# Kernel optimization log

Measured on AMD Instinct MI355X. Metric: run time of the kernel, lower is better.

## Reference

```python
import jax, jax.numpy as jnp
import numpy as np

B, N, E, H = 2, 256, 256, 768


def setup_inputs() -> dict:
    key = jax.random.key(0)
    ks = jax.random.split(key, 9)
    s_e = 1.0 / np.sqrt(E)
    s_h = 1.0 / np.sqrt(H)
    return {
        "x": jax.random.normal(ks[0], (B, N, E), dtype=jnp.float32),
        "Wq": jax.random.uniform(ks[1], (E, H), jnp.float32, -s_e, s_e),
        "bq": jax.random.uniform(ks[2], (H,), jnp.float32, -s_e, s_e),
        "Wk": jax.random.uniform(ks[3], (E, H), jnp.float32, -s_e, s_e),
        "bk": jax.random.uniform(ks[4], (H,), jnp.float32, -s_e, s_e),
        "Wv": jax.random.uniform(ks[5], (E, H), jnp.float32, -s_e, s_e),
        "bv": jax.random.uniform(ks[6], (H,), jnp.float32, -s_e, s_e),
        "we": jax.random.uniform(ks[7], (H,), jnp.float32, -s_h, s_h),
        "be": jax.random.uniform(ks[8], (), jnp.float32, -s_h, s_h),
    }


def reference(x, Wq, bq, Wk, bk, Wv, bv, we, be):
    # Projections: [B,N,H]
    q = x @ Wq + bq
    k = x @ Wk + bk
    v = x @ Wv + bv
    # Per (i,j): q_i + k_j + v_j  (key and value both broadcast over query axis)
    kv = k + v  # [B,N,H]
    # energy: [B,N,N] = leaky_relu(q_i + kv_j) . we + be
    energy = jnp.einsum(
        "bijh,h->bij",
        jax.nn.leaky_relu(q[:, :, None, :] + kv[:, None, :, :], negative_slope=0.01),
        we,
    ) + be
    attn = jax.nn.softmax(energy, axis=-1)  # softmax over keys j
    return jnp.einsum("bij,bjh->bih", attn, v)  # [B,N,H]
```

## Files before the change

### kernel.cpp

```cpp
#include <hip/hip_runtime.h>

#define B 2
#define N 256
#define E 256
#define H 768
#define H4 (H / 4)

__global__ __launch_bounds__(256) void proj_kernel(
    const float* __restrict__ x,
    const float* __restrict__ Wq, const float* __restrict__ bq,
    const float* __restrict__ Wk, const float* __restrict__ bk,
    const float* __restrict__ Wv, const float* __restrict__ bv,
    float* __restrict__ q, float* __restrict__ v, float4* __restrict__ kvT)
{
    __shared__ float  xs[E][8];
    __shared__ float4 red[8][4][64];

    const int t    = threadIdx.x;
    const int lane = t & 63;
    const int rg   = t >> 6;
    const int type = blockIdx.x / 192;
    const int bid  = blockIdx.x % 192;
    const int ct   = bid >> 6;
    const int rt   = bid & 63;
    const int r0   = rt * 8;
    const int c    = ct * 256 + lane * 4;

    {
        float4 lo, hi;
        lo.x = x[(r0 + 0) * E + t]; lo.y = x[(r0 + 1) * E + t];
        lo.z = x[(r0 + 2) * E + t]; lo.w = x[(r0 + 3) * E + t];
        hi.x = x[(r0 + 4) * E + t]; hi.y = x[(r0 + 5) * E + t];
        hi.z = x[(r0 + 6) * E + t]; hi.w = x[(r0 + 7) * E + t];
        *(float4*)&xs[t][0] = lo;
        *(float4*)&xs[t][4] = hi;
    }

    float4 bias;
    if (type == 0)       bias = *(const float4*)(bq + c);
    else if (type == 2)  bias = *(const float4*)(bv + c);
    else {
        const float4 p = *(const float4*)(bk + c);
        const float4 r = *(const float4*)(bv + c);
        bias.x = p.x + r.x; bias.y = p.y + r.y; bias.z = p.z + r.z; bias.w = p.w + r.w;
    }
    __syncthreads();

    const int e0 = rg * 64;
    float4 a0 = {0,0,0,0}, a1 = a0, a2 = a0, a3 = a0, a4 = a0, a5 = a0, a6 = a0, a7 = a0;

#define PROJ_STEP(ee, wv)                                                     \
    { const float4 xA = *(const float4*)&xs[ee][0];                           \
      const float4 xB = *(const float4*)&xs[ee][4];                           \
      a0.x = fmaf(xA.x, wv.x, a0.x); a0.y = fmaf(xA.x, wv.y, a0.y);           \
      a0.z = fmaf(xA.x, wv.z, a0.z); a0.w = fmaf(xA.x, wv.w, a0.w);           \
      a1.x = fmaf(xA.y, wv.x, a1.x); a1.y = fmaf(xA.y, wv.y, a1.y);           \
      a1.z = fmaf(xA.y, wv.z, a1.z); a1.w = fmaf(xA.y, wv.w, a1.w);           \
      a2.x = fmaf(xA.z, wv.x, a2.x); a2.y = fmaf(xA.z, wv.y, a2.y);           \
      a2.z = fmaf(xA.z, wv.z, a2.z); a2.w = fmaf(xA.z, wv.w, a2.w);           \
      a3.x = fmaf(xA.w, wv.x, a3.x); a3.y = fmaf(xA.w, wv.y, a3.y);           \
      a3.z = fmaf(xA.w, wv.z, a3.z); a3.w = fmaf(xA.w, wv.w, a3.w);           \
      a4.x = fmaf(xB.x, wv.x, a4.x); a4.y = fmaf(xB.x, wv.y, a4.y);           \
      a4.z = fmaf(xB.x, wv.z, a4.z); a4.w = fmaf(xB.x, wv.w, a4.w);           \
      a5.x = fmaf(xB.y, wv.x, a5.x); a5.y = fmaf(xB.y, wv.y, a5.y);           \
      a5.z = fmaf(xB.y, wv.z, a5.z); a5.w = fmaf(xB.y, wv.w, a5.w);           \
      a6.x = fmaf(xB.z, wv.x, a6.x); a6.y = fmaf(xB.z, wv.y, a6.y);           \
      a6.z = fmaf(xB.z, wv.z, a6.z); a6.w = fmaf(xB.z, wv.w, a6.w);           \
      a7.x = fmaf(xB.w, wv.x, a7.x); a7.y = fmaf(xB.w, wv.y, a7.y);           \
      a7.z = fmaf(xB.w, wv.z, a7.z); a7.w = fmaf(xB.w, wv.w, a7.w); }

    if (type == 1) {
        const float4* Wkp = (const float4*)(Wk + c);
        const float4* Wvp = (const float4*)(Wv + c);
        float4 k0 = Wkp[(e0 + 0) * H4], k1 = Wkp[(e0 + 1) * H4];
        float4 k2 = Wkp[(e0 + 2) * H4], k3 = Wkp[(e0 + 3) * H4];
        float4 u0 = Wvp[(e0 + 0) * H4], u1 = Wvp[(e0 + 1) * H4];
        float4 u2 = Wvp[(e0 + 2) * H4], u3 = Wvp[(e0 + 3) * H4];
        float4 s0, s1, s2, s3;
        s0.x=k0.x+u0.x; s0.y=k0.y+u0.y; s0.z=k0.z+u0.z; s0.w=k0.w+u0.w;
        s1.x=k1.x+u1.x; s1.y=k1.y+u1.y; s1.z=k1.z+u1.z; s1.w=k1.w+u1.w;
        s2.x=k2.x+u2.x; s2.y=k2.y+u2.y; s2.z=k2.z+u2.z; s2.w=k2.w+u2.w;
        s3.x=k3.x+u3.x; s3.y=k3.y+u3.y; s3.z=k3.z+u3.z; s3.w=k3.w+u3.w;
        int e = e0;
        #pragma unroll 1
        for (; e < e0 + 60; e += 4) {
            float4 nk0 = Wkp[(e + 4) * H4], nk1 = Wkp[(e + 5) * H4];
            float4 nk2 = Wkp[(e + 6) * H4], nk3 = Wkp[(e + 7) * H4];
            float4 nu0 = Wvp[(e + 4) * H4], nu1 = Wvp[(e + 5) * H4];
            float4 nu2 = Wvp[(e + 6) * H4], nu3 = Wvp[(e + 7) * H4];
            PROJ_STEP(e    , s0);
            PROJ_STEP(e + 1, s1);
            PROJ_STEP(e + 2, s2);
            PROJ_STEP(e + 3, s3);
            s0.x=nk0.x+nu0.x; s0.y=nk0.y+nu0.y; s0.z=nk0.z+nu0.z; s0.w=nk0.w+nu0.w;
            s1.x=nk1.x+nu1.x; s1.y=nk1.y+nu1.y; s1.z=nk1.z+nu1.z; s1.w=nk1.w+nu1.w;
            s2.x=nk2.x+nu2.x; s2.y=nk2.y+nu2.y; s2.z=nk2.z+nu2.z; s2.w=nk2.w+nu2.w;
            s3.x=nk3.x+nu3.x; s3.y=nk3.y+nu3.y; s3.z=nk3.z+nu3.z; s3.w=nk3.w+nu3.w;
        }
        PROJ_STEP(e    , s0);
        PROJ_STEP(e + 1, s1);
        PROJ_STEP(e + 2, s2);
        PROJ_STEP(e + 3, s3);
    } else {
        const float* W = (type == 0) ? Wq : Wv;
        const float4* Wp = (const float4*)(W + c);
        float4 w0 = Wp[(e0 + 0) * H4], w1 = Wp[(e0 + 1) * H4];
        float4 w2 = Wp[(e0 + 2) * H4], w3 = Wp[(e0 + 3) * H4];
        int e = e0;
        #pragma unroll 1
        for (; e < e0 + 60; e += 4) {
            float4 n0 = Wp[(e + 4) * H4], n1 = Wp[(e + 5) * H4];
            float4 n2 = Wp[(e + 6) * H4], n3 = Wp[(e + 7) * H4];
            PROJ_STEP(e    , w0);
            PROJ_STEP(e + 1, w1);
            PROJ_STEP(e + 2, w2);
            PROJ_STEP(e + 3, w3);
            w0 = n0; w1 = n1; w2 = n2; w3 = n3;
        }
        PROJ_STEP(e    , w0);
        PROJ_STEP(e + 1, w1);
        PROJ_STEP(e + 2, w2);
        PROJ_STEP(e + 3, w3);
    }
#undef PROJ_STEP

    red[0][rg][lane] = a0; red[1][rg][lane] = a1;
    red[2][rg][lane] = a2; red[3][rg][lane] = a3;
    red[4][rg][lane] = a4; red[5][rg][lane] = a5;
    red[6][rg][lane] = a6; red[7][rg][lane] = a7;
    __syncthreads();

    #pragma unroll
    for (int ri = 0; ri < 2; ++ri) {
        const int r = 2 * rg + ri;
        const float4 p0 = red[r][0][lane], p1 = red[r][1][lane];
        const float4 p2 = red[r][2][lane], p3 = red[r][3][lane];
        float4 s;
        s.x = ((p0.x + p1.x) + (p2.x + p3.x)) + bias.x;
        s.y = ((p0.y + p1.y) + (p2.y + p3.y)) + bias.y;
        s.z = ((p0.z + p1.z) + (p2.z + p3.z)) + bias.z;
        s.w = ((p0.w + p1.w) + (p2.w + p3.w)) + bias.w;
        const int row = r0 + r;
        if (type == 0) {
            *(float4*)(q + row * H + c) = s;
        } else if (type == 2) {
            *(float4*)(v + row * H + c) = s;
        } else {
            const int b = row >> 8, n = row & 255;
            kvT[(b * H4 + (c >> 2)) * N + n] = s;
        }
    }
}

__global__ __launch_bounds__(512) void energy_kernel(
    const float* __restrict__ q, const float4* __restrict__ kvT,
    const float* __restrict__ we, const float* __restrict__ be_p,
    float* __restrict__ eout)
{
    __shared__ float qs[8][H];
    __shared__ float wes[H];
    __shared__ float pE[8][8][64];

    const int t    = threadIdx.x;
    const int jl   = t & 63;
    const int hq   = t >> 6;
    const int row0 = (blockIdx.x >> 2) * 8;
    const int j0   = (blockIdx.x & 3) * 64;
    const int b    = row0 >> 8;

    for (int i = t; i < H; i += 512) {
        wes[i] = we[i];
        #pragma unroll
        for (int r = 0; r < 8; ++r) qs[r][i] = q[(row0 + r) * H + i];
    }
    __syncthreads();

    const float4* kvp = kvT + (size_t)b * H4 * N + (j0 + jl);
    const int base = hq * 24;

    float acc[8] = {0.f, 0.f, 0.f, 0.f, 0.f, 0.f, 0.f, 0.f};

#define ESTEP8(idx, kvv)                                                      \
    { const float4 ww = *(const float4*)&wes[(idx) * 4];                      \
      _Pragma("unroll")                                                       \
      for (int r = 0; r < 8; ++r) {                                           \
          const float4 qa = *(const float4*)&qs[r][(idx) * 4];                \
          float s;                                                            \
          s = qa.x + kvv.x; acc[r] = fmaf(fmaxf(s, 0.01f * s), ww.x, acc[r]); \
          s = qa.y + kvv.y; acc[r] = fmaf(fmaxf(s, 0.01f * s), ww.y, acc[r]); \
          s = qa.z + kvv.z; acc[r] = fmaf(fmaxf(s, 0.01f * s), ww.z, acc[r]); \
          s = qa.w + kvv.w; acc[r] = fmaf(fmaxf(s, 0.01f * s), ww.w, acc[r]); \
      } }

    float4 k0 = kvp[(base + 0) * N], k1 = kvp[(base + 1) * N];
    float4 k2 = kvp[(base + 2) * N], k3 = kvp[(base + 3) * N];
    int it = 0;
    #pragma unroll 1
    for (; it < 20; it += 4) {
        float4 n0 = kvp[(base + it + 4) * N], n1 = kvp[(base + it + 5) * N];
        float4 n2 = kvp[(base + it + 6) * N], n3 = kvp[(base + it + 7) * N];
        ESTEP8(base + it    , k0);
        ESTEP8(base + it + 1, k1);
        ESTEP8(base + it + 2, k2);
        ESTEP8(base + it + 3, k3);
        k0 = n0; k1 = n1; k2 = n2; k3 = n3;
    }
    ESTEP8(base + 20, k0);
    ESTEP8(base + 21, k1);
    ESTEP8(base + 22, k2);
    ESTEP8(base + 23, k3);
#undef ESTEP8

    #pragma unroll
    for (int r = 0; r < 8; ++r) pE[r][hq][jl] = acc[r];
    __syncthreads();

    const int rr = t >> 6;
    const float be = be_p[0];
    float ev = be;
    #pragma unroll
    for (int k = 0; k < 8; ++k) ev += pE[rr][k][jl];
    eout[(size_t)(row0 + rr) * N + j0 + jl] = ev;
}

#define PSTEP(aj, vv, Am) \
    Am.x = fmaf(aj, vv.x, Am.x); Am.y = fmaf(aj, vv.y, Am.y); \
    Am.z = fmaf(aj, vv.z, Am.z); Am.w = fmaf(aj, vv.w, Am.w);

__global__ __launch_bounds__(256) void pv_kernel(
    const float* __restrict__ eout, const float* __restrict__ v,
    float* __restrict__ out)
{
    __shared__ float es[8][256];
    __shared__ float inv_s[8];

    const int t   = threadIdx.x;
    const int b   = blockIdx.x / 192;
    const int r_  = blockIdx.x % 192;
    const int it_ = r_ / 6;
    const int ht  = r_ % 6;
    const int i0  = it_ * 8;
    const int h4l = t & 31;
    const int il  = t >> 5;

    {
        float4* es4 = (float4*)es;
        const float4* ep = (const float4*)(eout + (size_t)(b * 256 + i0) * N);
        es4[t]       = ep[t];
        es4[t + 256] = ep[t + 256];
    }
    __syncthreads();

    const int wv = t >> 6, ln = t & 63;
    #pragma unroll
    for (int rr = 0; rr < 2; ++rr) {
        const int row = wv * 2 + rr;
        const float4 evv = ((const float4*)es[row])[ln];
        float m = fmaxf(fmaxf(evv.x, evv.y), fmaxf(evv.z, evv.w));
        #pragma unroll
        for (int off = 1; off < 64; off <<= 1) m = fmaxf(m, __shfl_xor(m, off));
        float4 p;
        p.x = __expf(evv.x - m); p.y = __expf(evv.y - m);
        p.z = __expf(evv.z - m); p.w = __expf(evv.w - m);
        float s = (p.x + p.y) + (p.z + p.w);
        #pragma unroll
        for (int off = 1; off < 64; off <<= 1) s += __shfl_xor(s, off);
        ((float4*)es[row])[ln] = p;
        if (ln == 0) inv_s[row] = 1.0f / s;
    }
    __syncthreads();

    const float4* vp = (const float4*)(v + (size_t)(b * 256) * H + ht * 128) + h4l;
    const float4* a4 = (const float4*)es[il];

    float4 P = {0.f, 0.f, 0.f, 0.f}, Q = P;
    float4 av = a4[0];
    float4 v0 = vp[0], v1 = vp[H4], v2 = vp[2 * H4], v3 = vp[3 * H4];
    int j4 = 0;
    #pragma unroll 1
    for (; j4 < 63; ++j4) {
        const float4 nav = a4[j4 + 1];
        const int jb = 4 * j4 + 4;
        float4 n0 = vp[(jb + 0) * H4], n1 = vp[(jb + 1) * H4];
        float4 n2 = vp[(jb + 2) * H4], n3 = vp[(jb + 3) * H4];
        PSTEP(av.x, v0, P); PSTEP(av.y, v1, Q);
        PSTEP(av.z, v2, P); PSTEP(av.w, v3, Q);
        av = nav;
        v0 = n0; v1 = n1; v2 = n2; v3 = n3;
    }
    PSTEP(av.x, v0, P); PSTEP(av.y, v1, Q);
    PSTEP(av.z, v2, P); PSTEP(av.w, v3, Q);

    const float is = inv_s[il];
    float4 R;
    R.x = (P.x + Q.x) * is; R.y = (P.y + Q.y) * is;
    R.z = (P.z + Q.z) * is; R.w = (P.w + Q.w) * is;
    *(float4*)(out + (size_t)(b * 256 + i0 + il) * H + ht * 128 + h4l * 4) = R;
}

extern "C" void kernel_launch(void* const* d_in, const int* in_sizes, int n_in,
                              void* d_out, int out_size, void* d_ws, size_t ws_size,
                              hipStream_t stream) {
    const float* x  = (const float*)d_in[0];
    const float* Wq = (const float*)d_in[1];
    const float* bq = (const float*)d_in[2];
    const float* Wk = (const float*)d_in[3];
    const float* bk = (const float*)d_in[4];
    const float* Wv = (const float*)d_in[5];
    const float* bv = (const float*)d_in[6];
    const float* we = (const float*)d_in[7];
    const float* be = (const float*)d_in[8];
    float* out = (float*)d_out;

    float*  q    = (float*)d_ws;
    float*  v    = q + B * N * H;
    float4* kvT  = (float4*)(v + B * N * H);
    float*  eout = (float*)(kvT + B * H4 * N);

    proj_kernel<<<576, 256, 0, stream>>>(x, Wq, bq, Wk, bk, Wv, bv, q, v, kvT);
    energy_kernel<<<256, 512, 0, stream>>>(q, kvT, we, be, eout);
    pv_kernel<<<384, 256, 0, stream>>>(eout, v, out);
}
```

Baseline: 57.98 us.

## Rewrite leaky-relu energy as abs term plus softmax-invariant linear term

Leaky ReLU is decomposed as 0.505*s + 0.495*|s|. The per-query linear part and the scalar bias `be` are dropped because they cancel in the softmax. The per-key linear part (kv·we) is accumulated alongside, so the inner energy loop needs only add, abs and fma per element instead of add, mul, max and fma. The energy kernel now handles two key columns per thread with 16 H-groups. The projection kernel computes K and V in one block, sharing the x tile, and writes both v and k+v, which cuts the grid from 576 to 384 blocks. The cost is extra accumulator registers and one more reduction pass through shared memory, plus small float rounding differences from the reordered sums.

```diff
diff --git a/kernel.cpp b/kernel.cpp
--- a/kernel.cpp
+++ b/kernel.cpp
@@ -6,11 +6,32 @@
 #define H 768
 #define H4 (H / 4)
 
+#define PROJ_STEP(ee, wv, A)                                                  \
+    { const float4 xA = *(const float4*)&xs[ee][0];                           \
+      const float4 xB = *(const float4*)&xs[ee][4];                           \
+      A[0].x = fmaf(xA.x, wv.x, A[0].x); A[0].y = fmaf(xA.x, wv.y, A[0].y);   \
+      A[0].z = fmaf(xA.x, wv.z, A[0].z); A[0].w = fmaf(xA.x, wv.w, A[0].w);   \
+      A[1].x = fmaf(xA.y, wv.x, A[1].x); A[1].y = fmaf(xA.y, wv.y, A[1].y);   \
+      A[1].z = fmaf(xA.y, wv.z, A[1].z); A[1].w = fmaf(xA.y, wv.w, A[1].w);   \
+      A[2].x = fmaf(xA.z, wv.x, A[2].x); A[2].y = fmaf(xA.z, wv.y, A[2].y);   \
+      A[2].z = fmaf(xA.z, wv.z, A[2].z); A[2].w = fmaf(xA.z, wv.w, A[2].w);   \
+      A[3].x = fmaf(xA.w, wv.x, A[3].x); A[3].y = fmaf(xA.w, wv.y, A[3].y);   \
+      A[3].z = fmaf(xA.w, wv.z, A[3].z); A[3].w = fmaf(xA.w, wv.w, A[3].w);   \
+      A[4].x = fmaf(xB.x, wv.x, A[4].x); A[4].y = fmaf(xB.x, wv.y, A[4].y);   \
+      A[4].z = fmaf(xB.x, wv.z, A[4].z); A[4].w = fmaf(xB.x, wv.w, A[4].w);   \
+      A[5].x = fmaf(xB.y, wv.x, A[5].x); A[5].y = fmaf(xB.y, wv.y, A[5].y);   \
+      A[5].z = fmaf(xB.y, wv.z, A[5].z); A[5].w = fmaf(xB.y, wv.w, A[5].w);   \
+      A[6].x = fmaf(xB.z, wv.x, A[6].x); A[6].y = fmaf(xB.z, wv.y, A[6].y);   \
+      A[6].z = fmaf(xB.z, wv.z, A[6].z); A[6].w = fmaf(xB.z, wv.w, A[6].w);   \
+      A[7].x = fmaf(xB.w, wv.x, A[7].x); A[7].y = fmaf(xB.w, wv.y, A[7].y);   \
+      A[7].z = fmaf(xB.w, wv.z, A[7].z); A[7].w = fmaf(xB.w, wv.w, A[7].w); }
+
 __global__ __launch_bounds__(256) void proj_kernel(
     const float* __restrict__ x,
     const float* __restrict__ Wq, const float* __restrict__ bq,
     const float* __restrict__ Wk, const float* __restrict__ bk,
     const float* __restrict__ Wv, const float* __restrict__ bv,
+    const float* __restrict__ we, float* __restrict__ wb,
     float* __restrict__ q, float* __restrict__ v, float4* __restrict__ kvT)
 {
     __shared__ float  xs[E][8];
@@ -26,6 +47,12 @@
     const int r0   = rt * 8;
     const int c    = ct * 256 + lane * 4;
 
+    if (blockIdx.x == 0 && t < H4) {
+        float4 w = ((const float4*)we)[t];
+        w.x *= 0.495f; w.y *= 0.495f; w.z *= 0.495f; w.w *= 0.495f;
+        ((float4*)wb)[t] = w;
+    }
+
     {
         float4 lo, hi;
         lo.x = x[(r0 + 0) * E + t]; lo.y = x[(r0 + 1) * E + t];
@@ -35,75 +62,13 @@
         *(float4*)&xs[t][0] = lo;
         *(float4*)&xs[t][4] = hi;
     }
-
-    float4 bias;
-    if (type == 0)       bias = *(const float4*)(bq + c);
-    else if (type == 2)  bias = *(const float4*)(bv + c);
-    else {
-        const float4 p = *(const float4*)(bk + c);
-        const float4 r = *(const float4*)(bv + c);
-        bias.x = p.x + r.x; bias.y = p.y + r.y; bias.z = p.z + r.z; bias.w = p.w + r.w;
-    }
     __syncthreads();
 
     const int e0 = rg * 64;
-    float4 a0 = {0,0,0,0}, a1 = a0, a2 = a0, a3 = a0, a4 = a0, a5 = a0, a6 = a0, a7 = a0;
-
-#define PROJ_STEP(ee, wv)                                                     \
-    { const float4 xA = *(const float4*)&xs[ee][0];                           \
-      const float4 xB = *(const float4*)&xs[ee][4];                           \
-      a0.x = fmaf(xA.x, wv.x, a0.x); a0.y = fmaf(xA.x, wv.y, a0.y);           \
-      a0.z = fmaf(xA.x, wv.z, a0.z); a0.w = fmaf(xA.x, wv.w, a0.w);           \
-      a1.x = fmaf(xA.y, wv.x, a1.x); a1.y = fmaf(xA.y, wv.y, a1.y);           \
-      a1.z = fmaf(xA.y, wv.z, a1.z); a1.w = fmaf(xA.y, wv.w, a1.w);           \
-      a2.x = fmaf(xA.z, wv.x, a2.x); a2.y = fmaf(xA.z, wv.y, a2.y);           \
-      a2.z = fmaf(xA.z, wv.z, a2.z); a2.w = fmaf(xA.z, wv.w, a2.w);           \
-      a3.x = fmaf(xA.w, wv.x, a3.x); a3.y = fmaf(xA.w, wv.y, a3.y);           \
-      a3.z = fmaf(xA.w, wv.z, a3.z); a3.w = fmaf(xA.w, wv.w, a3.w);           \
-      a4.x = fmaf(xB.x, wv.x, a4.x); a4.y = fmaf(xB.x, wv.y, a4.y);           \
-      a4.z = fmaf(xB.x, wv.z, a4.z); a4.w = fmaf(xB.x, wv.w, a4.w);           \
-      a5.x = fmaf(xB.y, wv.x, a5.x); a5.y = fmaf(xB.y, wv.y, a5.y);           \
-      a5.z = fmaf(xB.y, wv.z, a5.z); a5.w = fmaf(xB.y, wv.w, a5.w);           \
-      a6.x = fmaf(xB.z, wv.x, a6.x); a6.y = fmaf(xB.z, wv.y, a6.y);           \
-      a6.z = fmaf(xB.z, wv.z, a6.z); a6.w = fmaf(xB.z, wv.w, a6.w);           \
-      a7.x = fmaf(xB.w, wv.x, a7.x); a7.y = fmaf(xB.w, wv.y, a7.y);           \
-      a7.z = fmaf(xB.w, wv.z, a7.z); a7.w = fmaf(xB.w, wv.w, a7.w); }
-
-    if (type == 1) {
-        const float4* Wkp = (const float4*)(Wk + c);
-        const float4* Wvp = (const float4*)(Wv + c);
-        float4 k0 = Wkp[(e0 + 0) * H4], k1 = Wkp[(e0 + 1) * H4];
-        float4 k2 = Wkp[(e0 + 2) * H4], k3 = Wkp[(e0 + 3) * H4];
-        float4 u0 = Wvp[(e0 + 0) * H4], u1 = Wvp[(e0 + 1) * H4];
-        float4 u2 = Wvp[(e0 + 2) * H4], u3 = Wvp[(e0 + 3) * H4];
-        float4 s0, s1, s2, s3;
-        s0.x=k0.x+u0.x; s0.y=k0.y+u0.y; s0.z=k0.z+u0.z; s0.w=k0.w+u0.w;
-        s1.x=k1.x+u1.x; s1.y=k1.y+u1.y; s1.z=k1.z+u1.z; s1.w=k1.w+u1.w;
-        s2.x=k2.x+u2.x; s2.y=k2.y+u2.y; s2.z=k2.z+u2.z; s2.w=k2.w+u2.w;
-        s3.x=k3.x+u3.x; s3.y=k3.y+u3.y; s3.z=k3.z+u3.z; s3.w=k3.w+u3.w;
-        int e = e0;
-        #pragma unroll 1
-        for (; e < e0 + 60; e += 4) {
-            float4 nk0 = Wkp[(e + 4) * H4], nk1 = Wkp[(e + 5) * H4];
-            float4 nk2 = Wkp[(e + 6) * H4], nk3 = Wkp[(e + 7) * H4];
-            float4 nu0 = Wvp[(e + 4) * H4], nu1 = Wvp[(e + 5) * H4];
-            float4 nu2 = Wvp[(e + 6) * H4], nu3 = Wvp[(e + 7) * H4];
-            PROJ_STEP(e    , s0);
-            PROJ_STEP(e + 1, s1);
-            PROJ_STEP(e + 2, s2);
-            PROJ_STEP(e + 3, s3);
-            s0.x=nk0.x+nu0.x; s0.y=nk0.y+nu0.y; s0.z=nk0.z+nu0.z; s0.w=nk0.w+nu0.w;
-            s1.x=nk1.x+nu1.x; s1.y=nk1.y+nu1.y; s1.z=nk1.z+nu1.z; s1.w=nk1.w+nu1.w;
-            s2.x=nk2.x+nu2.x; s2.y=nk2.y+nu2.y; s2.z=nk2.z+nu2.z; s2.w=nk2.w+nu2.w;
-            s3.x=nk3.x+nu3.x; s3.y=nk3.y+nu3.y; s3.z=nk3.z+nu3.z; s3.w=nk3.w+nu3.w;
-        }
-        PROJ_STEP(e    , s0);
-        PROJ_STEP(e + 1, s1);
-        PROJ_STEP(e + 2, s2);
-        PROJ_STEP(e + 3, s3);
-    } else {
-        const float* W = (type == 0) ? Wq : Wv;
-        const float4* Wp = (const float4*)(W + c);
+
+    if (type == 0) {
+        float4 A[8] = {};
+        const float4* Wp = (const float4*)(Wq + c);
         float4 w0 = Wp[(e0 + 0) * H4], w1 = Wp[(e0 + 1) * H4];
         float4 w2 = Wp[(e0 + 2) * H4], w3 = Wp[(e0 + 3) * H4];
         int e = e0;
@@ -111,116 +76,178 @@
         for (; e < e0 + 60; e += 4) {
             float4 n0 = Wp[(e + 4) * H4], n1 = Wp[(e + 5) * H4];
             float4 n2 = Wp[(e + 6) * H4], n3 = Wp[(e + 7) * H4];
-            PROJ_STEP(e    , w0);
-            PROJ_STEP(e + 1, w1);
-            PROJ_STEP(e + 2, w2);
-            PROJ_STEP(e + 3, w3);
+            PROJ_STEP(e    , w0, A);
+            PROJ_STEP(e + 1, w1, A);
+            PROJ_STEP(e + 2, w2, A);
+            PROJ_STEP(e + 3, w3, A);
             w0 = n0; w1 = n1; w2 = n2; w3 = n3;
         }
-        PROJ_STEP(e    , w0);
-        PROJ_STEP(e + 1, w1);
-        PROJ_STEP(e + 2, w2);
-        PROJ_STEP(e + 3, w3);
-    }
+        PROJ_STEP(e    , w0, A);
+        PROJ_STEP(e + 1, w1, A);
+        PROJ_STEP(e + 2, w2, A);
+        PROJ_STEP(e + 3, w3, A);
+
+        #pragma unroll
+        for (int r = 0; r < 8; ++r) red[r][rg][lane] = A[r];
+        __syncthreads();
+        const float4 bias = *(const float4*)(bq + c);
+        #pragma unroll
+        for (int ri = 0; ri < 2; ++ri) {
+            const int r = 2 * rg + ri;
+            const float4 p0 = red[r][0][lane], p1 = red[r][1][lane];
+            const float4 p2 = red[r][2][lane], p3 = red[r][3][lane];
+            float4 s;
+            s.x = ((p0.x + p1.x) + (p2.x + p3.x)) + bias.x;
+            s.y = ((p0.y + p1.y) + (p2.y + p3.y)) + bias.y;
+            s.z = ((p0.z + p1.z) + (p2.z + p3.z)) + bias.z;
+            s.w = ((p0.w + p1.w) + (p2.w + p3.w)) + bias.w;
+            *(float4*)(q + (size_t)(r0 + r) * H + c) = s;
+        }
+    } else {
+        float4 AK[8] = {}, AV[8] = {};
+        const float4* Kp = (const float4*)(Wk + c);
+        const float4* Vp = (const float4*)(Wv + c);
+        float4 k0 = Kp[(e0 + 0) * H4], k1 = Kp[(e0 + 1) * H4];
+        float4 u0 = Vp[(e0 + 0) * H4], u1 = Vp[(e0 + 1) * H4];
+        int e = e0;
+        #pragma unroll 1
+        for (; e < e0 + 62; e += 2) {
+            float4 nk0 = Kp[(e + 2) * H4], nk1 = Kp[(e + 3) * H4];
+            float4 nu0 = Vp[(e + 2) * H4], nu1 = Vp[(e + 3) * H4];
+            PROJ_STEP(e    , k0, AK);
+            PROJ_STEP(e    , u0, AV);
+            PROJ_STEP(e + 1, k1, AK);
+            PROJ_STEP(e + 1, u1, AV);
+            k0 = nk0; k1 = nk1; u0 = nu0; u1 = nu1;
+        }
+        PROJ_STEP(e    , k0, AK);
+        PROJ_STEP(e    , u0, AV);
+        PROJ_STEP(e + 1, k1, AK);
+        PROJ_STEP(e + 1, u1, AV);
+
+        #pragma unroll
+        for (int r = 0; r < 8; ++r) red[r][rg][lane] = AV[r];
+        __syncthreads();
+        const float4 bv4 = *(const float4*)(bv + c);
+        const float4 bk4 = *(const float4*)(bk + c);
+        float4 vs[2];
+        #pragma unroll
+        for (int ri = 0; ri < 2; ++ri) {
+            const int r = 2 * rg + ri;
+            const float4 p0 = red[r][0][lane], p1 = red[r][1][lane];
+            const float4 p2 = red[r][2][lane], p3 = red[r][3][lane];
+            float4 s;
+            s.x = ((p0.x + p1.x) + (p2.x + p3.x)) + bv4.x;
+            s.y = ((p0.y + p1.y) + (p2.y + p3.y)) + bv4.y;
+            s.z = ((p0.z + p1.z) + (p2.z + p3.z)) + bv4.z;
+            s.w = ((p0.w + p1.w) + (p2.w + p3.w)) + bv4.w;
+            vs[ri] = s;
+            *(float4*)(v + (size_t)(r0 + r) * H + c) = s;
+        }
+        __syncthreads();
+
+        #pragma unroll
+        for (int r = 0; r < 8; ++r) red[r][rg][lane] = AK[r];
+        __syncthreads();
+        #pragma unroll
+        for (int ri = 0; ri < 2; ++ri) {
+            const int r = 2 * rg + ri;
+            const float4 p0 = red[r][0][lane], p1 = red[r][1][lane];
+            const float4 p2 = red[r][2][lane], p3 = red[r][3][lane];
+            float4 s;
+            s.x = ((p0.x + p1.x) + (p2.x + p3.x)) + bk4.x + vs[ri].x;
+            s.y = ((p0.y + p1.y) + (p2.y + p3.y)) + bk4.y + vs[ri].y;
+            s.z = ((p0.z + p1.z) + (p2.z + p3.z)) + bk4.z + vs[ri].z;
+            s.w = ((p0.w + p1.w) + (p2.w + p3.w)) + bk4.w + vs[ri].w;
+            const int row = r0 + r;
+            const int bb = row >> 8, n = row & 255;
+            kvT[((size_t)bb * H4 + (c >> 2)) * N + n] = s;
+        }
+    }
+}
 #undef PROJ_STEP
-
-    red[0][rg][lane] = a0; red[1][rg][lane] = a1;
-    red[2][rg][lane] = a2; red[3][rg][lane] = a3;
-    red[4][rg][lane] = a4; red[5][rg][lane] = a5;
-    red[6][rg][lane] = a6; red[7][rg][lane] = a7;
-    __syncthreads();
-
-    #pragma unroll
-    for (int ri = 0; ri < 2; ++ri) {
-        const int r = 2 * rg + ri;
-        const float4 p0 = red[r][0][lane], p1 = red[r][1][lane];
-        const float4 p2 = red[r][2][lane], p3 = red[r][3][lane];
-        float4 s;
-        s.x = ((p0.x + p1.x) + (p2.x + p3.x)) + bias.x;
-        s.y = ((p0.y + p1.y) + (p2.y + p3.y)) + bias.y;
-        s.z = ((p0.z + p1.z) + (p2.z + p3.z)) + bias.z;
-        s.w = ((p0.w + p1.w) + (p2.w + p3.w)) + bias.w;
-        const int row = r0 + r;
-        if (type == 0) {
-            *(float4*)(q + row * H + c) = s;
-        } else if (type == 2) {
-            *(float4*)(v + row * H + c) = s;
-        } else {
-            const int b = row >> 8, n = row & 255;
-            kvT[(b * H4 + (c >> 2)) * N + n] = s;
-        }
-    }
-}
 
 __global__ __launch_bounds__(512) void energy_kernel(
     const float* __restrict__ q, const float4* __restrict__ kvT,
-    const float* __restrict__ we, const float* __restrict__ be_p,
-    float* __restrict__ eout)
+    const float* __restrict__ wb, float* __restrict__ eout)
 {
     __shared__ float qs[8][H];
-    __shared__ float wes[H];
-    __shared__ float pE[8][8][64];
+    __shared__ float wbs[H];
+    __shared__ float pE[8][16][64];
 
     const int t    = threadIdx.x;
-    const int jl   = t & 63;
-    const int hq   = t >> 6;
+    const int jl   = t & 31;
+    const int hq   = t >> 5;
     const int row0 = (blockIdx.x >> 2) * 8;
     const int j0   = (blockIdx.x & 3) * 64;
     const int b    = row0 >> 8;
 
-    for (int i = t; i < H; i += 512) {
-        wes[i] = we[i];
-        #pragma unroll
-        for (int r = 0; r < 8; ++r) qs[r][i] = q[(row0 + r) * H + i];
-    }
-    __syncthreads();
-
-    const float4* kvp = kvT + (size_t)b * H4 * N + (j0 + jl);
-    const int base = hq * 24;
-
-    float acc[8] = {0.f, 0.f, 0.f, 0.f, 0.f, 0.f, 0.f, 0.f};
-
-#define ESTEP8(idx, kvv)                                                      \
-    { const float4 ww = *(const float4*)&wes[(idx) * 4];                      \
-      _Pragma("unroll")                                                       \
-      for (int r = 0; r < 8; ++r) {                                           \
-          const float4 qa = *(const float4*)&qs[r][(idx) * 4];                \
-          float s;                                                            \
-          s = qa.x + kvv.x; acc[r] = fmaf(fmaxf(s, 0.01f * s), ww.x, acc[r]); \
-          s = qa.y + kvv.y; acc[r] = fmaf(fmaxf(s, 0.01f * s), ww.y, acc[r]); \
-          s = qa.z + kvv.z; acc[r] = fmaf(fmaxf(s, 0.01f * s), ww.z, acc[r]); \
-          s = qa.w + kvv.w; acc[r] = fmaf(fmaxf(s, 0.01f * s), ww.w, acc[r]); \
+    {
+        float4* qs4 = (float4*)qs;
+        const float4* qg = (const float4*)(q + (size_t)row0 * H);
+        #pragma unroll
+        for (int i = 0; i < 3; ++i) qs4[t + 512 * i] = qg[t + 512 * i];
+        if (t < H4) ((float4*)wbs)[t] = ((const float4*)wb)[t];
+    }
+    __syncthreads();
+
+    const float4* kv0 = kvT + (size_t)b * H4 * N + (j0 + jl);
+    const int base = hq * 12;
+
+    float acc0[8] = {0,0,0,0,0,0,0,0};
+    float acc1[8] = {0,0,0,0,0,0,0,0};
+    float4 ka0 = {0,0,0,0}, ka1 = {0,0,0,0};
+
+#define ESTEP2(idx, u0_, u1_)                                                   \
+    { const float4 wb4 = *(const float4*)&wbs[(idx) * 4];                       \
+      ka0.x = fmaf(u0_.x, wb4.x, ka0.x); ka0.y = fmaf(u0_.y, wb4.y, ka0.y);     \
+      ka0.z = fmaf(u0_.z, wb4.z, ka0.z); ka0.w = fmaf(u0_.w, wb4.w, ka0.w);     \
+      ka1.x = fmaf(u1_.x, wb4.x, ka1.x); ka1.y = fmaf(u1_.y, wb4.y, ka1.y);     \
+      ka1.z = fmaf(u1_.z, wb4.z, ka1.z); ka1.w = fmaf(u1_.w, wb4.w, ka1.w);     \
+      _Pragma("unroll")                                                         \
+      for (int r = 0; r < 8; ++r) {                                             \
+          const float4 qa = *(const float4*)&qs[r][(idx) * 4];                  \
+          float s;                                                              \
+          s = qa.x + u0_.x; acc0[r] = fmaf(__builtin_fabsf(s), wb4.x, acc0[r]); \
+          s = qa.x + u1_.x; acc1[r] = fmaf(__builtin_fabsf(s), wb4.x, acc1[r]); \
+          s = qa.y + u0_.y; acc0[r] = fmaf(__builtin_fabsf(s), wb4.y, acc0[r]); \
+          s = qa.y + u1_.y; acc1[r] = fmaf(__builtin_fabsf(s), wb4.y, acc1[r]); \
+          s = qa.z + u0_.z; acc0[r] = fmaf(__builtin_fabsf(s), wb4.z, acc0[r]); \
+          s = qa.z + u1_.z; acc1[r] = fmaf(__builtin_fabsf(s), wb4.z, acc1[r]); \
+          s = qa.w + u0_.w; acc0[r] = fmaf(__builtin_fabsf(s), wb4.w, acc0[r]); \
+          s = qa.w + u1_.w; acc1[r] = fmaf(__builtin_fabsf(s), wb4.w, acc1[r]); \
       } }
 
-    float4 k0 = kvp[(base + 0) * N], k1 = kvp[(base + 1) * N];
-    float4 k2 = kvp[(base + 2) * N], k3 = kvp[(base + 3) * N];
+    float4 a0 = kv0[(base + 0) * N],      a1 = kv0[(base + 1) * N];
+    float4 c0 = kv0[(base + 0) * N + 32], c1 = kv0[(base + 1) * N + 32];
     int it = 0;
     #pragma unroll 1
-    for (; it < 20; it += 4) {
-        float4 n0 = kvp[(base + it + 4) * N], n1 = kvp[(base + it + 5) * N];
-        float4 n2 = kvp[(base + it + 6) * N], n3 = kvp[(base + it + 7) * N];
-        ESTEP8(base + it    , k0);
-        ESTEP8(base + it + 1, k1);
-        ESTEP8(base + it + 2, k2);
-        ESTEP8(base + it + 3, k3);
-        k0 = n0; k1 = n1; k2 = n2; k3 = n3;
-    }
-    ESTEP8(base + 20, k0);
-    ESTEP8(base + 21, k1);
-    ESTEP8(base + 22, k2);
-    ESTEP8(base + 23, k3);
-#undef ESTEP8
-
+    for (; it < 10; it += 2) {
+        float4 na0 = kv0[(base + it + 2) * N],      na1 = kv0[(base + it + 3) * N];
+        float4 nc0 = kv0[(base + it + 2) * N + 32], nc1 = kv0[(base + it + 3) * N + 32];
+        ESTEP2(base + it    , a0, c0);
+        ESTEP2(base + it + 1, a1, c1);
+        a0 = na0; a1 = na1; c0 = nc0; c1 = nc1;
+    }
+    ESTEP2(base + 10, a0, c0);
+    ESTEP2(base + 11, a1, c1);
+#undef ESTEP2
+
+    const float KS = 0.505f / 0.495f;
+    const float k0s = KS * ((ka0.x + ka0.y) + (ka0.z + ka0.w));
+    const float k1s = KS * ((ka1.x + ka1.y) + (ka1.z + ka1.w));
     #pragma unroll
-    for (int r = 0; r < 8; ++r) pE[r][hq][jl] = acc[r];
-    __syncthreads();
-
-    const int rr = t >> 6;
-    const float be = be_p[0];
-    float ev = be;
+    for (int r = 0; r < 8; ++r) {
+        pE[r][hq][jl]      = acc0[r] + k0s;
+        pE[r][hq][jl + 32] = acc1[r] + k1s;
+    }
+    __syncthreads();
+
+    const int rr = t >> 6, jc = t & 63;
+    float ev = 0.f;
     #pragma unroll
-    for (int k = 0; k < 8; ++k) ev += pE[rr][k][jl];
-    eout[(size_t)(row0 + rr) * N + j0 + jl] = ev;
+    for (int k = 0; k < 16; ++k) ev += pE[rr][k][jc];
+    eout[(size_t)(row0 + rr) * N + j0 + jc] = ev;
 }
 
 #define PSTEP(aj, vv, Am) \
@@ -309,15 +336,15 @@
     const float* Wv = (const float*)d_in[5];
     const float* bv = (const float*)d_in[6];
     const float* we = (const float*)d_in[7];
-    const float* be = (const float*)d_in[8];
     float* out = (float*)d_out;
 
     float*  q    = (float*)d_ws;
     float*  v    = q + B * N * H;
     float4* kvT  = (float4*)(v + B * N * H);
     float*  eout = (float*)(kvT + B * H4 * N);
-
-    proj_kernel<<<576, 256, 0, stream>>>(x, Wq, bq, Wk, bk, Wv, bv, q, v, kvT);
-    energy_kernel<<<256, 512, 0, stream>>>(q, kvT, we, be, eout);
+    float*  wb   = eout + B * N * N;
+
+    proj_kernel<<<384, 256, 0, stream>>>(x, Wq, bq, Wk, bk, Wv, bv, we, wb, q, v, kvT);
+    energy_kernel<<<256, 512, 0, stream>>>(q, kvT, wb, eout);
     pv_kernel<<<384, 256, 0, stream>>>(eout, v, out);
 }
```

Measured after the change: 56.69 us. 2.2% less time.
